# Kernel optimization log

Hardware: AMD Instinct MI355X
Metric: run time of the kernel (lower is better)

The kernel has to match this reference:

```python
import jax, jax.numpy as jnp
import numpy as np

N = 131072   # nodes
C = 128      # in_channels
R = 4        # num_residues
H = 128      # hidden_channels
B = 1024     # graphs (segments)
QS = jnp.arange(1, 10, dtype=jnp.float32) * 0.1  # quantiles 0.1..0.9


def setup_inputs() -> dict:
    key = jax.random.key(0)
    ks = jax.random.split(key, 12)
    s = 0.05
    return {
        "embedding_0": jax.random.normal(ks[0], (N, C, 1, R), jnp.float32),
        "batch": jnp.sort(jax.random.randint(ks[1], (N,), 0, B, dtype=jnp.int32)),
        "W_lins": jax.random.normal(ks[2], (R - 1, C), jnp.float32) * s,
        "b_lins": jax.random.normal(ks[3], (R - 1,), jnp.float32) * s,
        "W1": jax.random.normal(ks[4], (C, H), jnp.float32) * s,
        "b1": jax.random.normal(ks[5], (H,), jnp.float32) * s,
        "W2": jax.random.normal(ks[6], (H,), jnp.float32) * s,
        "b2": jax.random.normal(ks[7], (1,), jnp.float32) * s,
        "Wm1": jax.random.normal(ks[8], (12, H), jnp.float32) * s,
        "bm1": jax.random.normal(ks[9], (H,), jnp.float32) * s,
        "Wm2": jax.random.normal(ks[10], (H,), jnp.float32) * s,
        "bm2": jax.random.normal(ks[11], (1,), jnp.float32) * s,
    }


def _node_readout(emb, W_lins, b_lins, W1, b1, W2, b2):
    x = emb[:, :, 0, :]                         # [N, C, R]
    # sum of (num_residues-1) plain linears, each Linear(C, 1)
    lin = jnp.einsum('ncr,rc->n', x[:, :, :-1], W_lins) + jnp.sum(b_lins)
    # non-linear branch on last residue: Linear(C,H) -> relu -> Linear(H,1)
    h = jax.nn.relu(x[:, :, -1] @ W1 + b1)      # [N, H]
    nl = h @ W2 + b2                            # [N]
    return lin + nl                             # [N]


def _multi_aggregate(v, batch):
    ones = jnp.ones_like(v)
    counts_f = jax.ops.segment_sum(ones, batch, num_segments=B)        # [B]
    counts = counts_f.astype(jnp.int32)
    safe_cnt = jnp.maximum(counts_f, 1.0)
    mean = jax.ops.segment_sum(v, batch, num_segments=B) / safe_cnt
    mx = jax.ops.segment_max(v, batch, num_segments=B)
    mn = jax.ops.segment_min(v, batch, num_segments=B)
    # per-segment sort (batch is primary key, value secondary)
    order = jnp.lexsort((v, batch))
    vs = v[order]                                                      # segment-sorted values
    offsets = jnp.concatenate([jnp.zeros(1, jnp.int32), jnp.cumsum(counts)[:-1].astype(jnp.int32)])
    last = offsets + jnp.maximum(counts, 1) - 1                        # last valid index per segment
    # linear-interpolated quantiles: pos = q*(count-1) within each segment
    pos = QS[:, None] * (safe_cnt[None, :] - 1.0)                      # [9, B]
    f = jnp.floor(pos).astype(jnp.int32)
    frac = pos - f.astype(jnp.float32)
    lo_idx = jnp.clip(offsets[None, :] + f, offsets[None, :], last[None, :])
    hi_idx = jnp.clip(lo_idx + 1, offsets[None, :], last[None, :])
    quant = vs[lo_idx] + frac * (vs[hi_idx] - vs[lo_idx])              # [9, B]
    nonempty = (counts > 0)[:, None]
    agg = jnp.concatenate([mean[:, None], mx[:, None], mn[:, None], quant.T], axis=1)  # [B, 12]
    return jnp.where(nonempty, agg, 0.0)


def reference(embedding_0, batch, W_lins, b_lins, W1, b1, W2, b2, Wm1, bm1, Wm2, bm2):
    batch = batch.astype(jnp.int32)
    v = _node_readout(embedding_0, W_lins, b_lins, W1, b1, W2, b2)     # [N]
    agg = _multi_aggregate(v, batch)                                   # [B, 12]
    out = jax.nn.relu(agg @ Wm1 + bm1) @ Wm2 + bm2                     # [B]
    return out
```

## Files before the change

### kernel.cpp

```cpp
#include <hip/hip_runtime.h>

#define N_NODES 131072
#define C_DIM   128
#define H_DIM   128
#define B_SEG   1024
#define M_TILE  128
#define K_TILE  32
#define YT_STR  132
#define SEGCAP  384

__global__ __launch_bounds__(256, 4)
void node_readout_kernel(const float* __restrict__ emb,
                         const float* __restrict__ W_lins,
                         const float* __restrict__ b_lins,
                         const float* __restrict__ W1,
                         const float* __restrict__ b1,
                         const float* __restrict__ W2,
                         const float* __restrict__ b2,
                         float* __restrict__ v_out)
{
    __shared__ float Yt[K_TILE * YT_STR];
    __shared__ float W1s[K_TILE * H_DIM];
    __shared__ float WLs[3 * C_DIM];
    __shared__ float lin_lds[M_TILE];

    const int t  = threadIdx.x;
    const int nbase = blockIdx.x * M_TILE;
    const int ln = t >> 5;
    const int cc = t & 31;
    const int jg = t & 15;
    const int mg = t >> 4;

    for (int i = t; i < 3 * C_DIM; i += 256) WLs[i] = W_lins[i];

    float acc[8][8];
    #pragma unroll
    for (int mi = 0; mi < 8; ++mi)
        #pragma unroll
        for (int ji = 0; ji < 8; ++ji) acc[mi][ji] = 0.0f;

    float lin_p[16];
    #pragma unroll
    for (int p = 0; p < 16; ++p) lin_p[p] = 0.0f;

    const float4* xbase = (const float4*)emb + (size_t)(nbase + ln) * C_DIM;

    __syncthreads();

    for (int ct = 0; ct < C_DIM / K_TILE; ++ct) {
        if (ct) __syncthreads();

        {
            const float4* src = (const float4*)(W1 + ct * K_TILE * H_DIM);
            float4* dst = (float4*)W1s;
            #pragma unroll
            for (int i = 0; i < 4; ++i) dst[t + 256 * i] = src[t + 256 * i];
        }
        {
            const int c0 = ct * K_TILE + cc;
            #pragma unroll
            for (int p = 0; p < 16; ++p) {
                float4 x = xbase[p * 8 * C_DIM + ct * K_TILE + cc];
                lin_p[p] += x.x * WLs[c0] + x.y * WLs[C_DIM + c0] + x.z * WLs[2 * C_DIM + c0];
                Yt[cc * YT_STR + p * 8 + ln] = x.w;
            }
        }
        __syncthreads();

        #pragma unroll 8
        for (int k = 0; k < K_TILE; ++k) {
            float4 ya = *(const float4*)&Yt[k * YT_STR + mg * 8];
            float4 yb = *(const float4*)&Yt[k * YT_STR + mg * 8 + 4];
            float w[8];
            #pragma unroll
            for (int ji = 0; ji < 8; ++ji) w[ji] = W1s[k * H_DIM + jg + 16 * ji];
            float ym[8] = {ya.x, ya.y, ya.z, ya.w, yb.x, yb.y, yb.z, yb.w};
            #pragma unroll
            for (int mi = 0; mi < 8; ++mi)
                #pragma unroll
                for (int ji = 0; ji < 8; ++ji)
                    acc[mi][ji] = fmaf(ym[mi], w[ji], acc[mi][ji]);
        }
    }

    #pragma unroll
    for (int p = 0; p < 16; ++p) {
        float s = lin_p[p];
        s += __shfl_xor(s, 16);
        s += __shfl_xor(s, 8);
        s += __shfl_xor(s, 4);
        s += __shfl_xor(s, 2);
        s += __shfl_xor(s, 1);
        lin_p[p] = s;
    }
    if (cc == 0) {
        #pragma unroll
        for (int p = 0; p < 16; ++p) lin_lds[p * 8 + ln] = lin_p[p];
    }

    __syncthreads();
    float* nl_red = W1s;

    float b1r[8], W2r[8];
    #pragma unroll
    for (int ji = 0; ji < 8; ++ji) {
        int j = jg + 16 * ji;
        b1r[ji] = b1[j];
        W2r[ji] = W2[j];
    }

    #pragma unroll
    for (int mi = 0; mi < 8; ++mi) {
        float s = 0.0f;
        #pragma unroll
        for (int ji = 0; ji < 8; ++ji) {
            float h = acc[mi][ji] + b1r[ji];
            h = h > 0.0f ? h : 0.0f;
            s = fmaf(h, W2r[ji], s);
        }
        nl_red[(mg * 8 + mi) * 17 + jg] = s;
    }
    __syncthreads();

    if (t < M_TILE) {
        float s = lin_lds[t];
        #pragma unroll
        for (int g = 0; g < 16; ++g) s += nl_red[t * 17 + g];
        s += b_lins[0] + b_lins[1] + b_lins[2] + b2[0];
        v_out[nbase + t] = s;
    }
}

__global__ __launch_bounds__(256)
void aggregate_kernel(const float* __restrict__ v,
                      const int* __restrict__ batch,
                      const float* __restrict__ Wm1,
                      const float* __restrict__ bm1,
                      const float* __restrict__ Wm2,
                      const float* __restrict__ bm2,
                      float* __restrict__ out)
{
    __shared__ float vals[4][SEGCAP];
    __shared__ float sorted[4][SEGCAP];
    __shared__ float agg_s[4][12];

    const int t    = threadIdx.x;
    const int wid  = t >> 6;
    const int lane = t & 63;
    const int b    = blockIdx.x * 4 + wid;

    int lo = 0, hi = N_NODES;
    while (lo < hi) { int mid = (lo + hi) >> 1; if (batch[mid] < b) lo = mid + 1; else hi = mid; }
    const int start = lo;
    hi = N_NODES;
    while (lo < hi) { int mid = (lo + hi) >> 1; if (batch[mid] <= b) lo = mid + 1; else hi = mid; }
    int cnt = lo - start;
    if (cnt > SEGCAP) cnt = SEGCAP;

    float lsum = 0.0f;
    for (int i = lane; i < cnt; i += 64) {
        float x = v[start + i];
        vals[wid][i] = x;
        lsum += x;
    }
    #pragma unroll
    for (int o = 32; o; o >>= 1) lsum += __shfl_xor(lsum, o);
    __syncthreads();

    for (int i = lane; i < cnt; i += 64) {
        float xi = vals[wid][i];
        int r = 0;
        for (int j = 0; j < cnt; ++j) {
            float xj = vals[wid][j];
            r += (xj < xi) || (xj == xi && j < i);
        }
        sorted[wid][r] = xi;
    }
    __syncthreads();

    if (cnt > 0) {
        float cntf = (float)cnt;
        if (lane == 9)  agg_s[wid][0] = lsum / cntf;
        if (lane == 10) agg_s[wid][1] = sorted[wid][cnt - 1];
        if (lane == 11) agg_s[wid][2] = sorted[wid][0];
        if (lane < 9) {
            float q   = (float)(lane + 1) * 0.1f;
            float pos = q * (cntf - 1.0f);
            float f   = floorf(pos);
            float frac = pos - f;
            int loi = (int)f;
            int hii = loi + 1; if (hii > cnt - 1) hii = cnt - 1;
            agg_s[wid][3 + lane] = sorted[wid][loi] + frac * (sorted[wid][hii] - sorted[wid][loi]);
        }
    } else {
        if (lane < 12) agg_s[wid][lane] = 0.0f;
    }
    __syncthreads();

    float term = 0.0f;
    #pragma unroll
    for (int rj = 0; rj < 2; ++rj) {
        int j = lane + 64 * rj;
        float h = bm1[j];
        #pragma unroll
        for (int k = 0; k < 12; ++k) h = fmaf(agg_s[wid][k], Wm1[k * H_DIM + j], h);
        h = h > 0.0f ? h : 0.0f;
        term = fmaf(h, Wm2[j], term);
    }
    #pragma unroll
    for (int o = 32; o; o >>= 1) term += __shfl_xor(term, o);
    if (lane == 0) out[b] = term + bm2[0];
}

extern "C" void kernel_launch(void* const* d_in, const int* in_sizes, int n_in,
                              void* d_out, int out_size, void* d_ws, size_t ws_size,
                              hipStream_t stream)
{
    const float* emb    = (const float*)d_in[0];
    const int*   batch  = (const int*)d_in[1];
    const float* W_lins = (const float*)d_in[2];
    const float* b_lins = (const float*)d_in[3];
    const float* W1     = (const float*)d_in[4];
    const float* b1     = (const float*)d_in[5];
    const float* W2     = (const float*)d_in[6];
    const float* b2     = (const float*)d_in[7];
    const float* Wm1    = (const float*)d_in[8];
    const float* bm1    = (const float*)d_in[9];
    const float* Wm2    = (const float*)d_in[10];
    const float* bm2    = (const float*)d_in[11];

    float* out = (float*)d_out;
    float* vbuf = (float*)d_ws;

    node_readout_kernel<<<N_NODES / M_TILE, 256, 0, stream>>>(
        emb, W_lins, b_lins, W1, b1, W2, b2, vbuf);
    aggregate_kernel<<<B_SEG / 4, 256, 0, stream>>>(
        vbuf, batch, Wm1, bm1, Wm2, bm2, out);
}
```

Baseline: 501.2 us.

## Double-buffer node readout tiles with register prefetch and vectorized W1 LDS reads

The node readout GEMM now uses K-tiles of 16 with double-buffered shared memory. The next tile of embeddings and W1 is prefetched into registers while the current tile is computed, which needs one barrier per tile instead of two. W1 is stored in a padded row layout so each thread reads its 8 contiguous hidden columns with two float4 LDS loads instead of 8 scalar loads. The cost is more LDS and registers, with occupancy lowered to 3 blocks per CU, and the hidden-column mapping for b1/W2 changes to match.

New measurement: 1.518 ms. +202.8%, slower.

```diff
diff --git a/kernel.cpp b/kernel.cpp
--- a/kernel.cpp
+++ b/kernel.cpp
@@ -5,11 +5,13 @@
 #define H_DIM   128
 #define B_SEG   1024
 #define M_TILE  128
-#define K_TILE  32
-#define YT_STR  132
+#define KT      16
+#define NTILES  8
+#define ROWSTR  132
+#define TILE_F  (KT * ROWSTR)
 #define SEGCAP  384
 
-__global__ __launch_bounds__(256, 4)
+__global__ __launch_bounds__(256, 3)
 void node_readout_kernel(const float* __restrict__ emb,
                          const float* __restrict__ W_lins,
                          const float* __restrict__ b_lins,
@@ -19,17 +21,16 @@
                          const float* __restrict__ b2,
                          float* __restrict__ v_out)
 {
-    __shared__ float Yt[K_TILE * YT_STR];
-    __shared__ float W1s[K_TILE * H_DIM];
+    __shared__ float smem[4 * TILE_F];
     __shared__ float WLs[3 * C_DIM];
     __shared__ float lin_lds[M_TILE];
 
-    const int t  = threadIdx.x;
+    const int t     = threadIdx.x;
     const int nbase = blockIdx.x * M_TILE;
-    const int ln = t >> 5;
-    const int cc = t & 31;
-    const int jg = t & 15;
-    const int mg = t >> 4;
+    const int cc    = t & 15;
+    const int ln    = t >> 4;
+    const int jg    = t & 15;
+    const int mg    = t >> 4;
 
     for (int i = t; i < 3 * C_DIM; i += 256) WLs[i] = W_lins[i];
 
@@ -39,72 +40,112 @@
         #pragma unroll
         for (int ji = 0; ji < 8; ++ji) acc[mi][ji] = 0.0f;
 
-    float lin_p[16];
-    #pragma unroll
-    for (int p = 0; p < 16; ++p) lin_p[p] = 0.0f;
-
-    const float4* xbase = (const float4*)emb + (size_t)(nbase + ln) * C_DIM;
-
-    __syncthreads();
-
-    for (int ct = 0; ct < C_DIM / K_TILE; ++ct) {
-        if (ct) __syncthreads();
+    float lin_p[8];
+    #pragma unroll
+    for (int p = 0; p < 8; ++p) lin_p[p] = 0.0f;
+
+    const float4* emb4 = (const float4*)emb;
+    const float4* W1_4 = (const float4*)W1;
+
+    float4 xr[8];
+    float4 wr[2];
+
+    #pragma unroll
+    for (int p = 0; p < 8; ++p)
+        xr[p] = emb4[(size_t)(nbase + p * 16 + ln) * C_DIM + cc];
+    wr[0] = W1_4[t];
+    wr[1] = W1_4[t + 256];
+
+    __syncthreads();
+
+    {
+        float* yt = smem;
+        float* ws = smem + 2 * TILE_F;
+        const int c0 = cc;
+        const float wl0 = WLs[c0], wl1 = WLs[C_DIM + c0], wl2 = WLs[2 * C_DIM + c0];
+        #pragma unroll
+        for (int p = 0; p < 8; ++p) {
+            float4 x = xr[p];
+            lin_p[p] = fmaf(x.x, wl0, fmaf(x.y, wl1, fmaf(x.z, wl2, lin_p[p])));
+            yt[cc * ROWSTR + p * 16 + ln] = x.w;
+        }
+        #pragma unroll
+        for (int i = 0; i < 2; ++i) {
+            int gi = t + 256 * i;
+            int k = gi >> 5, g = gi & 31;
+            *(float4*)&ws[k * ROWSTR + 4 * (g + (g >> 4))] = wr[i];
+        }
+    }
+
+    const int wOff = 8 * jg + 4 * (jg >> 3);
+
+    for (int ct = 0; ct < NTILES; ++ct) {
+        __syncthreads();
+
+        if (ct < NTILES - 1) {
+            #pragma unroll
+            for (int p = 0; p < 8; ++p)
+                xr[p] = emb4[(size_t)(nbase + p * 16 + ln) * C_DIM + (ct + 1) * KT + cc];
+            wr[0] = W1_4[(ct + 1) * 512 + t];
+            wr[1] = W1_4[(ct + 1) * 512 + t + 256];
+        }
 
         {
-            const float4* src = (const float4*)(W1 + ct * K_TILE * H_DIM);
-            float4* dst = (float4*)W1s;
-            #pragma unroll
-            for (int i = 0; i < 4; ++i) dst[t + 256 * i] = src[t + 256 * i];
-        }
-        {
-            const int c0 = ct * K_TILE + cc;
-            #pragma unroll
-            for (int p = 0; p < 16; ++p) {
-                float4 x = xbase[p * 8 * C_DIM + ct * K_TILE + cc];
-                lin_p[p] += x.x * WLs[c0] + x.y * WLs[C_DIM + c0] + x.z * WLs[2 * C_DIM + c0];
-                Yt[cc * YT_STR + p * 8 + ln] = x.w;
+            const float* yt = smem + (ct & 1) * TILE_F;
+            const float* ws = smem + (2 + (ct & 1)) * TILE_F;
+            #pragma unroll
+            for (int k = 0; k < KT; ++k) {
+                float4 ya = *(const float4*)&yt[k * ROWSTR + mg * 8];
+                float4 yb = *(const float4*)&yt[k * ROWSTR + mg * 8 + 4];
+                float4 wa = *(const float4*)&ws[k * ROWSTR + wOff];
+                float4 wb = *(const float4*)&ws[k * ROWSTR + wOff + 4];
+                float ym[8] = {ya.x, ya.y, ya.z, ya.w, yb.x, yb.y, yb.z, yb.w};
+                float wv[8] = {wa.x, wa.y, wa.z, wa.w, wb.x, wb.y, wb.z, wb.w};
+                #pragma unroll
+                for (int mi = 0; mi < 8; ++mi)
+                    #pragma unroll
+                    for (int ji = 0; ji < 8; ++ji)
+                        acc[mi][ji] = fmaf(ym[mi], wv[ji], acc[mi][ji]);
             }
         }
-        __syncthreads();
-
-        #pragma unroll 8
-        for (int k = 0; k < K_TILE; ++k) {
-            float4 ya = *(const float4*)&Yt[k * YT_STR + mg * 8];
-            float4 yb = *(const float4*)&Yt[k * YT_STR + mg * 8 + 4];
-            float w[8];
-            #pragma unroll
-            for (int ji = 0; ji < 8; ++ji) w[ji] = W1s[k * H_DIM + jg + 16 * ji];
-            float ym[8] = {ya.x, ya.y, ya.z, ya.w, yb.x, yb.y, yb.z, yb.w};
-            #pragma unroll
-            for (int mi = 0; mi < 8; ++mi)
-                #pragma unroll
-                for (int ji = 0; ji < 8; ++ji)
-                    acc[mi][ji] = fmaf(ym[mi], w[ji], acc[mi][ji]);
-        }
-    }
-
-    #pragma unroll
-    for (int p = 0; p < 16; ++p) {
+
+        if (ct < NTILES - 1) {
+            float* yt = smem + ((ct + 1) & 1) * TILE_F;
+            float* ws = smem + (2 + ((ct + 1) & 1)) * TILE_F;
+            const int c0 = (ct + 1) * KT + cc;
+            const float wl0 = WLs[c0], wl1 = WLs[C_DIM + c0], wl2 = WLs[2 * C_DIM + c0];
+            #pragma unroll
+            for (int p = 0; p < 8; ++p) {
+                float4 x = xr[p];
+                lin_p[p] = fmaf(x.x, wl0, fmaf(x.y, wl1, fmaf(x.z, wl2, lin_p[p])));
+                yt[cc * ROWSTR + p * 16 + ln] = x.w;
+            }
+            #pragma unroll
+            for (int i = 0; i < 2; ++i) {
+                int gi = t + 256 * i;
+                int k = gi >> 5, g = gi & 31;
+                *(float4*)&ws[k * ROWSTR + 4 * (g + (g >> 4))] = wr[i];
+            }
+        }
+    }
+
+    #pragma unroll
+    for (int p = 0; p < 8; ++p) {
         float s = lin_p[p];
-        s += __shfl_xor(s, 16);
         s += __shfl_xor(s, 8);
         s += __shfl_xor(s, 4);
         s += __shfl_xor(s, 2);
         s += __shfl_xor(s, 1);
-        lin_p[p] = s;
-    }
-    if (cc == 0) {
-        #pragma unroll
-        for (int p = 0; p < 16; ++p) lin_lds[p * 8 + ln] = lin_p[p];
-    }
-
-    __syncthreads();
-    float* nl_red = W1s;
+        if (cc == 0) lin_lds[p * 16 + ln] = s;
+    }
+
+    __syncthreads();
+    float* nl_red = smem;
 
     float b1r[8], W2r[8];
     #pragma unroll
     for (int ji = 0; ji < 8; ++ji) {
-        int j = jg + 16 * ji;
+        int j = 8 * jg + ji;
         b1r[ji] = b1[j];
         W2r[ji] = W2[j];
     }
@@ -229,7 +270,7 @@
     const float* Wm2    = (const float*)d_in[10];
     const float* bm2    = (const float*)d_in[11];
 
-    float* out = (float*)d_out;
+    float* out  = (float*)d_out;
     float* vbuf = (float*)d_ws;
 
     node_readout_kernel<<<N_NODES / M_TILE, 256, 0, stream>>>(
```
